# Optimization experiments

Hardware: AMD Instinct MI355X
Metric: run time of the kernel (lower is better)

Reference implementation:

```python
import jax, jax.numpy as jnp
import numpy as np

NUM_EXPERTS = 8
D_MODEL = 1024
HIDDEN = 3 * D_MODEL
TOP_K = 2
LAMBDA = 0.01


def setup_inputs() -> dict:
    key = jax.random.key(0)
    k_x, k_w1, k_w2, k_r = jax.random.split(key, 4)
    B, T, C = 4, 2048, D_MODEL
    x = jax.random.normal(k_x, (B, T, C), dtype=jnp.float32)
    # per-expert SwishFFN weights (bias=False): W1 [E, C, H], W2 [E, H, C]
    W1 = jax.random.normal(k_w1, (NUM_EXPERTS, C, HIDDEN), dtype=jnp.float32) * (1.0 / np.sqrt(C))
    W2 = jax.random.normal(k_w2, (NUM_EXPERTS, HIDDEN, C), dtype=jnp.float32) * (1.0 / np.sqrt(HIDDEN))
    # router projection [C, E]
    Wr = jax.random.normal(k_r, (C, NUM_EXPERTS), dtype=jnp.float32) * (1.0 / np.sqrt(C))
    return {"x": x, "W1": W1, "W2": W2, "Wr": Wr}


def reference(x, W1, W2, Wr):
    B, T, C = x.shape
    E = W1.shape[0]
    xf = x.reshape(-1, C)                       # [N, C], N = B*T
    N = xf.shape[0]

    # Router: softmax over experts, keep top-k, renormalize among the k
    logits = xf @ Wr                            # [N, E]
    all_probs = jax.nn.softmax(logits, axis=-1)
    vals, idx = jax.lax.top_k(all_probs, TOP_K)  # [N, K]
    vals = vals / jnp.sum(vals, axis=-1, keepdims=True)
    routing_weight = jnp.zeros((N, E), dtype=xf.dtype).at[
        jnp.arange(N)[:, None], idx
    ].set(vals)                                  # sparse [N, E]

    # Expert combine: sum_e w_e * FFN_e(x); w_e == 0 for non-selected tokens,
    # so this equals the original masked gather/scatter loop exactly.
    out = jnp.zeros_like(xf)
    for e in range(E):
        h = jax.nn.silu(xf @ W1[e])              # [N, H]
        out = out + routing_weight[:, e:e + 1] * (h @ W2[e])

    # Load-balancing aux loss (fi detached)
    fi = jax.lax.stop_gradient(
        jnp.mean((routing_weight > 0).astype(xf.dtype), axis=0))
    pi = jnp.mean(all_probs, axis=0)
    aux_loss = LAMBDA * E * jnp.sum(fi * pi)

    return out.reshape(B, T, C), aux_loss
```

## Files before the change

### kernel.cpp

```cpp
#include <hip/hip_runtime.h>
#include <stdint.h>

#define N_TOK 8192
#define C_DIM 1024
#define H_DIM 3072
#define N_EXP 8
#define N_ASSIGN (N_TOK * 2)

typedef __attribute__((ext_vector_type(8))) short short8;
typedef __attribute__((ext_vector_type(4))) float f32x4;

__device__ __forceinline__ unsigned short f2bf(float f) {
    union { float f; uint32_t u; } v; v.f = f;
    uint32_t r = (v.u + 0x7FFFu + ((v.u >> 16) & 1u)) >> 16;
    return (unsigned short)r;
}

#define GLDS16(SRC, DST) __builtin_amdgcn_global_load_lds( \
    (const __attribute__((address_space(1))) void*)(SRC),  \
    (__attribute__((address_space(3))) void*)(DST), 16, 0, 0)

#define SBAR() do { __builtin_amdgcn_sched_barrier(0); \
    __builtin_amdgcn_s_barrier();                      \
    __builtin_amdgcn_sched_barrier(0); } while (0)

#define VM_WAIT(S) do { __builtin_amdgcn_sched_barrier(0); \
    asm volatile(S ::: "memory");                          \
    __builtin_amdgcn_sched_barrier(0); } while (0)

__global__ __launch_bounds__(256) void transpose_bf16_kernel(const float* __restrict__ in,
                                                             unsigned short* __restrict__ out,
                                                             int rows, int cols) {
    __shared__ float tile[64][65];
    int e = blockIdx.z;
    const float* ip = in + (size_t)e * rows * cols;
    unsigned short* op = out + (size_t)e * rows * cols;
    int c0 = blockIdx.x * 64;
    int r0 = blockIdx.y * 64;
    int t = threadIdx.x;
    int lr = t >> 4, lc4 = t & 15;
#pragma unroll
    for (int it = 0; it < 4; it++) {
        int r = lr + it * 16;
        float4 v = *(const float4*)&ip[(size_t)(r0 + r) * cols + c0 + lc4 * 4];
        tile[lc4 * 4 + 0][r] = v.x;
        tile[lc4 * 4 + 1][r] = v.y;
        tile[lc4 * 4 + 2][r] = v.z;
        tile[lc4 * 4 + 3][r] = v.w;
    }
    __syncthreads();
#pragma unroll
    for (int it = 0; it < 4; it++) {
        int oc = lr + it * 16;
        ushort4 o;
        o.x = f2bf(tile[oc][lc4 * 4 + 0]);
        o.y = f2bf(tile[oc][lc4 * 4 + 1]);
        o.z = f2bf(tile[oc][lc4 * 4 + 2]);
        o.w = f2bf(tile[oc][lc4 * 4 + 3]);
        *(ushort4*)&op[(size_t)(c0 + oc) * rows + r0 + lc4 * 4] = o;
    }
}

__global__ __launch_bounds__(256) void router_kernel(const float* __restrict__ x, const float* __restrict__ Wr,
                                                     int2* __restrict__ idx2, float2* __restrict__ wgt2,
                                                     float* __restrict__ piAcc, int* __restrict__ cntAcc) {
    __shared__ float s_pi[8];
    __shared__ int s_cnt[8];
    int t = threadIdx.x;
    if (t < 8) { s_pi[t] = 0.f; s_cnt[t] = 0; }
    __syncthreads();
    int lane = t & 63;
    int wid = t >> 6;
    int gwv = blockIdx.x * 4 + wid;
    int nw = gridDim.x * 4;
    for (int n = gwv; n < N_TOK; n += nw) {
        float acc[8];
#pragma unroll
        for (int e = 0; e < 8; e++) acc[e] = 0.f;
        const float* xr = x + (size_t)n * C_DIM;
#pragma unroll
        for (int j = 0; j < 16; j++) {
            int k = lane + 64 * j;
            float xv = xr[k];
            const float4* wr4 = (const float4*)(Wr + (size_t)k * 8);
            float4 a = wr4[0], b = wr4[1];
            acc[0] += xv * a.x; acc[1] += xv * a.y; acc[2] += xv * a.z; acc[3] += xv * a.w;
            acc[4] += xv * b.x; acc[5] += xv * b.y; acc[6] += xv * b.z; acc[7] += xv * b.w;
        }
#pragma unroll
        for (int off = 1; off < 64; off <<= 1) {
#pragma unroll
            for (int e = 0; e < 8; e++) acc[e] += __shfl_xor(acc[e], off, 64);
        }
        float m = acc[0];
#pragma unroll
        for (int e = 1; e < 8; e++) m = fmaxf(m, acc[e]);
        float p[8]; float s = 0.f;
#pragma unroll
        for (int e = 0; e < 8; e++) { p[e] = __expf(acc[e] - m); s += p[e]; }
        float inv = 1.f / s;
#pragma unroll
        for (int e = 0; e < 8; e++) p[e] *= inv;
        int i0 = 0; float l0 = acc[0];
#pragma unroll
        for (int e = 1; e < 8; e++) if (acc[e] > l0) { l0 = acc[e]; i0 = e; }
        int i1 = -1; float l1 = -1e30f;
#pragma unroll
        for (int e = 0; e < 8; e++) if (e != i0 && acc[e] > l1) { l1 = acc[e]; i1 = e; }
        if (lane == 0) {
            float v0 = p[i0], v1 = p[i1];
            float rs = 1.f / (v0 + v1);
            idx2[n] = make_int2(i0, i1);
            wgt2[n] = make_float2(v0 * rs, v1 * rs);
            atomicAdd(&s_cnt[i0], 1);
            atomicAdd(&s_cnt[i1], 1);
#pragma unroll
            for (int e = 0; e < 8; e++) atomicAdd(&s_pi[e], p[e]);
        }
    }
    __syncthreads();
    if (t < 8) { atomicAdd(&piAcc[t], s_pi[t]); atomicAdd(&cntAcc[t], s_cnt[t]); }
}

__global__ void finalize_router_kernel(const int* __restrict__ cnt, const float* __restrict__ pi,
                                       int* __restrict__ off, float* __restrict__ aux_out) {
    if (threadIdx.x == 0) {
        int o = 0;
        float dot = 0.f;
        for (int e = 0; e < 8; e++) {
            off[e] = o;
            o += cnt[e];
            dot += (float)cnt[e] * pi[e];
        }
        aux_out[0] = 0.01f * 8.f * dot / ((float)N_TOK * (float)N_TOK);
    }
}

__global__ __launch_bounds__(256) void scatter_kernel(const int2* __restrict__ idx2, const float2* __restrict__ wgt2,
                                                      const int* __restrict__ off, int* __restrict__ cursor,
                                                      int* __restrict__ tok, float* __restrict__ gwArr) {
    __shared__ int lcnt[8], lbase[8];
    int t = threadIdx.x;
    if (t < 8) lcnt[t] = 0;
    __syncthreads();
    int a = blockIdx.x * 256 + t;
    int n = a >> 1, k = a & 1;
    int2 id = idx2[n];
    float2 w = wgt2[n];
    int e = k ? id.y : id.x;
    float wv = k ? w.y : w.x;
    int rank = atomicAdd(&lcnt[e], 1);
    __syncthreads();
    if (t < 8) lbase[t] = atomicAdd(&cursor[t], lcnt[t]);
    __syncthreads();
    int pos = off[e] + lbase[e] + rank;
    tok[pos] = n;
    gwArr[pos] = wv;
}

__global__ __launch_bounds__(256) void gather_kernel(const float* __restrict__ x, const int* __restrict__ tok,
                                                     unsigned short* __restrict__ xg) {
    int wid = threadIdx.x >> 6, lane = threadIdx.x & 63;
    int row = blockIdx.x * 4 + wid;
    int n = tok[row];
    const float4* src = (const float4*)(x + (size_t)n * C_DIM);
    ushort4* dst = (ushort4*)(xg + (size_t)row * C_DIM);
#pragma unroll
    for (int j = 0; j < 4; j++) {
        float4 v = src[lane + 64 * j];
        ushort4 o;
        o.x = f2bf(v.x); o.y = f2bf(v.y); o.z = f2bf(v.z); o.w = f2bf(v.w);
        dst[lane + 64 * j] = o;
    }
}

template <int EPI>
__global__ __launch_bounds__(512) void moe_gemm_kernel(
    const unsigned short* __restrict__ A, int ldA,
    const unsigned short* __restrict__ Bt, int ldB, int bRowOff, int bColOff,
    int Kseg, int NY, int SK,
    const int* __restrict__ cnt, const int* __restrict__ off,
    const int* __restrict__ tok, const float* __restrict__ gwArr,
    unsigned short* __restrict__ hs, int ldH,
    float* __restrict__ out) {
    __shared__ unsigned short smem[65536];

    int nbs[8];
    int tot = 0;
#pragma unroll
    for (int i = 0; i < 8; i++) {
        nbs[i] = (cnt[i] + 255) >> 8;
        tot += nbs[i] * NY * SK;
    }
    int p = blockIdx.x;
    int q = tot >> 3, r = tot & 7;
    int xx = p & 7, sp = p >> 3;
    int capx = (xx < r) ? q + 1 : q;
    if (sp >= capx) return;
    int wi = (xx < r) ? xx * (q + 1) + sp : r * (q + 1) + (xx - r) * q + sp;

    int base = 0, e = -1, enb = 0, local = 0;
#pragma unroll
    for (int i = 0; i < 8; i++) {
        int sz = nbs[i] * NY * SK;
        if (e < 0 && wi < base + sz) { e = i; enb = nbs[i]; local = wi - base; }
        base += sz;
    }
    if (e < 0) return;
    int ys = local / enb;
    int mblk = local - ys * enb;
    int s = ys / NY;
    int y = ys - s * NY;
    int M = cnt[e];
    int m0 = mblk * 256;
    int baseRow = off[e];
    int n0 = y * 256;
    int acol = s * Kseg;
    int bcol = bColOff + s * Kseg;

    int tid = threadIdx.x;
    int lane = tid & 63;
    int wid = tid >> 6;
    int wm = (wid >> 2) * 128;
    int wn = (wid & 3) * 64;

    f32x4 acc[8][4];
#pragma unroll
    for (int i = 0; i < 8; i++)
#pragma unroll
        for (int j = 0; j < 4; j++) acc[i][j] = (f32x4)0.f;

    const unsigned short* Bex = Bt + (size_t)e * (size_t)(C_DIM * H_DIM);

    const unsigned short* srcA[2];
    const unsigned short* srcB[2];
    int ldsOff[2];
#pragma unroll
    for (int i = 0; i < 2; i++) {
        int c = i * 512 + tid;
        int row = c >> 2;
        int pos = c & 3;
        int sc = pos ^ ((row >> 1) & 3);
        int rg = m0 + row; if (rg > M - 1) rg = M - 1;
        srcA[i] = A + (size_t)(baseRow + rg) * ldA + acol + sc * 8;
        srcB[i] = Bex + (size_t)(bRowOff + n0 + row) * ldB + bcol + sc * 8;
        ldsOff[i] = (c & ~63) * 8;
    }

    int kq = lane >> 4;
    int rsub = lane & 15;
    int offA[8], offB[4];
#pragma unroll
    for (int m = 0; m < 8; m++) {
        int rr = wm + m * 16 + rsub;
        offA[m] = rr * 32 + ((kq ^ ((rr >> 1) & 3)) * 8);
    }
#pragma unroll
    for (int n = 0; n < 4; n++) {
        int rn = wn + n * 16 + rsub;
        offB[n] = 8192 + rn * 32 + ((kq ^ ((rn >> 1) & 3)) * 8);
    }

    int nt = Kseg >> 5;
#pragma unroll
    for (int tt = 0; tt < 3; tt++) {
#pragma unroll
        for (int i = 0; i < 2; i++) GLDS16(srcA[i], &smem[tt * 16384 + ldsOff[i]]);
#pragma unroll
        for (int i = 0; i < 2; i++) GLDS16(srcB[i], &smem[tt * 16384 + 8192 + ldsOff[i]]);
#pragma unroll
        for (int i = 0; i < 2; i++) { srcA[i] += 32; srcB[i] += 32; }
    }

#pragma unroll 1
    for (int t = 0; t < nt; ++t) {
        if (t < nt - 2)      VM_WAIT("s_waitcnt vmcnt(8)");
        else if (t == nt - 2) VM_WAIT("s_waitcnt vmcnt(4)");
        else                 VM_WAIT("s_waitcnt vmcnt(0)");
        SBAR();
        const unsigned short* buf = &smem[(t & 3) * 16384];
        short8 a[8], b[4];
#pragma unroll
        for (int m = 0; m < 8; m++) a[m] = *(const short8*)&buf[offA[m]];
#pragma unroll
        for (int n = 0; n < 4; n++) b[n] = *(const short8*)&buf[offB[n]];
        if (t + 3 < nt) {
            int bb = ((t + 3) & 3) * 16384;
#pragma unroll
            for (int i = 0; i < 2; i++) GLDS16(srcA[i], &smem[bb + ldsOff[i]]);
#pragma unroll
            for (int i = 0; i < 2; i++) GLDS16(srcB[i], &smem[bb + 8192 + ldsOff[i]]);
#pragma unroll
            for (int i = 0; i < 2; i++) { srcA[i] += 32; srcB[i] += 32; }
        }
        __builtin_amdgcn_s_setprio(1);
#pragma unroll
        for (int m = 0; m < 8; m++)
#pragma unroll
            for (int n = 0; n < 4; n++)
                acc[m][n] = __builtin_amdgcn_mfma_f32_16x16x32_bf16(a[m], b[n], acc[m][n], 0, 0, 0);
        __builtin_amdgcn_s_setprio(0);
    }

    int gRow = (lane >> 4) * 4;
    int cLane = lane & 15;
#pragma unroll
    for (int m = 0; m < 8; m++) {
#pragma unroll
        for (int j = 0; j < 4; j++) {
            int rr = m0 + wm + m * 16 + gRow + j;
            if (rr < M) {
                if (EPI == 0) {
#pragma unroll
                    for (int n = 0; n < 4; n++) {
                        int c = n0 + wn + n * 16 + cLane;
                        float v = acc[m][n][j];
                        float sv = v / (1.f + __expf(-v));
                        hs[(size_t)(baseRow + rr) * ldH + c] = f2bf(sv);
                    }
                } else {
                    int token = tok[baseRow + rr];
                    float w = gwArr[baseRow + rr];
#pragma unroll
                    for (int n = 0; n < 4; n++) {
                        int c = n0 + wn + n * 16 + cLane;
                        atomicAdd(&out[(size_t)token * C_DIM + c], w * acc[m][n][j]);
                    }
                }
            }
        }
    }
}

extern "C" void kernel_launch(void* const* d_in, const int* in_sizes, int n_in,
                              void* d_out, int out_size, void* d_ws, size_t ws_size,
                              hipStream_t stream) {
    const float* x = (const float*)d_in[0];
    const float* W1 = (const float*)d_in[1];
    const float* W2 = (const float*)d_in[2];
    const float* Wr = (const float*)d_in[3];
    float* out = (float*)d_out;

    char* p = (char*)d_ws;
    auto alloc = [&](size_t bytes) {
        char* r = p;
        p += (bytes + 255) & ~(size_t)255;
        return r;
    };
    float* pi = (float*)alloc(8 * sizeof(float));
    int* cntA = (int*)alloc(8 * sizeof(int));
    int* cursor = (int*)alloc(8 * sizeof(int));
    int* offA = (int*)alloc(8 * sizeof(int));
    int2* idx2 = (int2*)alloc((size_t)N_TOK * sizeof(int2));
    float2* wgt2 = (float2*)alloc((size_t)N_TOK * sizeof(float2));
    int* tok = (int*)alloc((size_t)N_ASSIGN * sizeof(int));
    float* gwA = (float*)alloc((size_t)N_ASSIGN * sizeof(float));
    unsigned short* W1bT = (unsigned short*)alloc((size_t)N_EXP * C_DIM * H_DIM * 2);
    unsigned short* W2bT = (unsigned short*)alloc((size_t)N_EXP * C_DIM * H_DIM * 2);
    unsigned short* xg = (unsigned short*)alloc((size_t)N_ASSIGN * C_DIM * 2);
    size_t used = (size_t)(p - (char*)d_ws);
    size_t remain = ws_size > used ? ws_size - used : 0;
    int HC = H_DIM;
    while (HC > 768 && (size_t)N_ASSIGN * HC * 2 > remain) HC >>= 1;
    unsigned short* hs = (unsigned short*)p;

    hipMemsetAsync(d_ws, 0, 1024, stream);
    hipMemsetAsync(d_out, 0, (size_t)N_TOK * C_DIM * sizeof(float), stream);

    transpose_bf16_kernel<<<dim3(H_DIM / 64, C_DIM / 64, N_EXP), 256, 0, stream>>>(W1, W1bT, C_DIM, H_DIM);
    transpose_bf16_kernel<<<dim3(C_DIM / 64, H_DIM / 64, N_EXP), 256, 0, stream>>>(W2, W2bT, H_DIM, C_DIM);

    router_kernel<<<256, 256, 0, stream>>>(x, Wr, idx2, wgt2, pi, cntA);
    finalize_router_kernel<<<1, 64, 0, stream>>>(cntA, pi, offA, out + (size_t)N_TOK * C_DIM);
    scatter_kernel<<<N_ASSIGN / 256, 256, 0, stream>>>(idx2, wgt2, offA, cursor, tok, gwA);
    gather_kernel<<<N_ASSIGN / 4, 256, 0, stream>>>(x, tok, xg);

    int nChunks = H_DIM / HC;
    for (int ci = 0; ci < nChunks; ++ci) {
        int h0 = ci * HC;
        int ny1 = HC / 256;
        int sk2 = (HC % 768 == 0) ? 3 : 2;
        moe_gemm_kernel<0><<<dim3(71 * ny1 + 8, 1, 1), 512, 0, stream>>>(
            xg, C_DIM, W1bT, C_DIM, h0, 0, C_DIM, ny1, 1,
            cntA, offA, tok, gwA, hs, HC, out);
        moe_gemm_kernel<1><<<dim3(71 * 4 * sk2 + 8, 1, 1), 512, 0, stream>>>(
            hs, HC, W2bT, H_DIM, 0, h0, HC / sk2, 4, sk2,
            cntA, offA, tok, gwA, hs, HC, out);
    }
}
```

Measured before the change: 506.7 us.

## Retile MoE GEMM to 256x128 with BK=64 triple buffer and interleaved loads

Shrinks the per-block output tile from 256x256 to 256x128 and doubles the K step to 64. The pipeline moves to a 3-stage LDS ring with an 8-chunk XOR swizzle. Global-to-LDS loads are split into pieces interleaved between four MFMA phases, separated by barriers and explicit lgkmcnt waits. The aim is better overlap of memory and MFMA work, fewer LDS bank conflicts, and more blocks for load balancing. The cost is lower arithmetic intensity per block (more B/A reloads), more barriers per iteration, and a changed split-K factor for the second GEMM.

```diff
diff --git a/kernel.cpp b/kernel.cpp
--- a/kernel.cpp
+++ b/kernel.cpp
@@ -24,7 +24,7 @@
     __builtin_amdgcn_s_barrier();                      \
     __builtin_amdgcn_sched_barrier(0); } while (0)
 
-#define VM_WAIT(S) do { __builtin_amdgcn_sched_barrier(0); \
+#define WAITASM(S) do { __builtin_amdgcn_sched_barrier(0); \
     asm volatile(S ::: "memory");                          \
     __builtin_amdgcn_sched_barrier(0); } while (0)
 
@@ -183,7 +183,7 @@
     const int* __restrict__ tok, const float* __restrict__ gwArr,
     unsigned short* __restrict__ hs, int ldH,
     float* __restrict__ out) {
-    __shared__ unsigned short smem[65536];
+    __shared__ unsigned short smem[73728];
 
     int nbs[8];
     int tot = 0;
@@ -214,92 +214,165 @@
     int M = cnt[e];
     int m0 = mblk * 256;
     int baseRow = off[e];
-    int n0 = y * 256;
+    int n0 = y * 128;
     int acol = s * Kseg;
     int bcol = bColOff + s * Kseg;
 
     int tid = threadIdx.x;
     int lane = tid & 63;
     int wid = tid >> 6;
-    int wm = (wid >> 2) * 128;
-    int wn = (wid & 3) * 64;
-
-    f32x4 acc[8][4];
+    int wr = wid >> 2;
+    int wc = wid & 3;
+
+    f32x4 acc[8][2];
 #pragma unroll
     for (int i = 0; i < 8; i++)
 #pragma unroll
-        for (int j = 0; j < 4; j++) acc[i][j] = (f32x4)0.f;
+        for (int j = 0; j < 2; j++) acc[i][j] = (f32x4)0.f;
 
     const unsigned short* Bex = Bt + (size_t)e * (size_t)(C_DIM * H_DIM);
 
-    const unsigned short* srcA[2];
+    const unsigned short* srcA[4];
     const unsigned short* srcB[2];
-    int ldsOff[2];
+    int ldsA[4], ldsB[2];
+#pragma unroll
+    for (int i = 0; i < 4; i++) {
+        int c = i * 512 + tid;
+        int row = c >> 3;
+        int sc = (c & 7) ^ (row & 7);
+        int rg = m0 + row; if (rg > M - 1) rg = M - 1;
+        srcA[i] = A + (size_t)(baseRow + rg) * ldA + acol + sc * 8;
+        ldsA[i] = (c & ~63) * 8;
+    }
 #pragma unroll
     for (int i = 0; i < 2; i++) {
         int c = i * 512 + tid;
-        int row = c >> 2;
-        int pos = c & 3;
-        int sc = pos ^ ((row >> 1) & 3);
-        int rg = m0 + row; if (rg > M - 1) rg = M - 1;
-        srcA[i] = A + (size_t)(baseRow + rg) * ldA + acol + sc * 8;
+        int row = c >> 3;
+        int sc = (c & 7) ^ (row & 7);
         srcB[i] = Bex + (size_t)(bRowOff + n0 + row) * ldB + bcol + sc * 8;
-        ldsOff[i] = (c & ~63) * 8;
+        ldsB[i] = 16384 + (c & ~63) * 8;
     }
 
     int kq = lane >> 4;
     int rsub = lane & 15;
-    int offA[8], offB[4];
-#pragma unroll
-    for (int m = 0; m < 8; m++) {
-        int rr = wm + m * 16 + rsub;
-        offA[m] = rr * 32 + ((kq ^ ((rr >> 1) & 3)) * 8);
-    }
-#pragma unroll
-    for (int n = 0; n < 4; n++) {
-        int rn = wn + n * 16 + rsub;
-        offB[n] = 8192 + rn * 32 + ((kq ^ ((rn >> 1) & 3)) * 8);
-    }
-
-    int nt = Kseg >> 5;
-#pragma unroll
-    for (int tt = 0; tt < 3; tt++) {
-#pragma unroll
-        for (int i = 0; i < 2; i++) GLDS16(srcA[i], &smem[tt * 16384 + ldsOff[i]]);
-#pragma unroll
-        for (int i = 0; i < 2; i++) GLDS16(srcB[i], &smem[tt * 16384 + 8192 + ldsOff[i]]);
-#pragma unroll
-        for (int i = 0; i < 2; i++) { srcA[i] += 32; srcB[i] += 32; }
-    }
-
+    int offA[2][8], offB[2][2];
+#pragma unroll
+    for (int kk = 0; kk < 2; kk++) {
+#pragma unroll
+        for (int m = 0; m < 8; m++) {
+            int row = wr * 128 + m * 16 + rsub;
+            offA[kk][m] = row * 64 + (((kk * 4 + kq) ^ (row & 7)) * 8);
+        }
+#pragma unroll
+        for (int n = 0; n < 2; n++) {
+            int col = wc * 32 + n * 16 + rsub;
+            offB[kk][n] = 16384 + col * 64 + (((kk * 4 + kq) ^ (col & 7)) * 8);
+        }
+    }
+
+    int nt = Kseg >> 6;
+#pragma unroll
+    for (int tt = 0; tt < 2; tt++) {
+        int bb = tt * 24576;
+#pragma unroll
+        for (int i = 0; i < 4; i++) { GLDS16(srcA[i], &smem[bb + ldsA[i]]); srcA[i] += 64; }
+#pragma unroll
+        for (int i = 0; i < 2; i++) { GLDS16(srcB[i], &smem[bb + ldsB[i]]); srcB[i] += 64; }
+    }
+
+    int bufR = 0, bufW = 2 * 24576;
 #pragma unroll 1
     for (int t = 0; t < nt; ++t) {
-        if (t < nt - 2)      VM_WAIT("s_waitcnt vmcnt(8)");
-        else if (t == nt - 2) VM_WAIT("s_waitcnt vmcnt(4)");
-        else                 VM_WAIT("s_waitcnt vmcnt(0)");
-        SBAR();
-        const unsigned short* buf = &smem[(t & 3) * 16384];
-        short8 a[8], b[4];
-#pragma unroll
-        for (int m = 0; m < 8; m++) a[m] = *(const short8*)&buf[offA[m]];
-#pragma unroll
-        for (int n = 0; n < 4; n++) b[n] = *(const short8*)&buf[offB[n]];
-        if (t + 3 < nt) {
-            int bb = ((t + 3) & 3) * 16384;
-#pragma unroll
-            for (int i = 0; i < 2; i++) GLDS16(srcA[i], &smem[bb + ldsOff[i]]);
-#pragma unroll
-            for (int i = 0; i < 2; i++) GLDS16(srcB[i], &smem[bb + 8192 + ldsOff[i]]);
-#pragma unroll
-            for (int i = 0; i < 2; i++) { srcA[i] += 32; srcB[i] += 32; }
-        }
+        const unsigned short* bp = &smem[bufR];
+        bool ds = (t + 2 < nt);
+        short8 a0, a1, a2, a3, b0, b1;
+        if (ds) {
+            GLDS16(srcA[0], &smem[bufW + ldsA[0]]); srcA[0] += 64;
+            GLDS16(srcA[1], &smem[bufW + ldsA[1]]); srcA[1] += 64;
+        }
+        if (t < nt - 2)       WAITASM("s_waitcnt vmcnt(8)");
+        else if (t == nt - 2) WAITASM("s_waitcnt vmcnt(6)");
+        else                  WAITASM("s_waitcnt vmcnt(0)");
+        SBAR();
+        a0 = *(const short8*)&bp[offA[0][0]];
+        a1 = *(const short8*)&bp[offA[0][1]];
+        a2 = *(const short8*)&bp[offA[0][2]];
+        a3 = *(const short8*)&bp[offA[0][3]];
+        b0 = *(const short8*)&bp[offB[0][0]];
+        b1 = *(const short8*)&bp[offB[0][1]];
+        WAITASM("s_waitcnt lgkmcnt(0)");
         __builtin_amdgcn_s_setprio(1);
-#pragma unroll
-        for (int m = 0; m < 8; m++)
-#pragma unroll
-            for (int n = 0; n < 4; n++)
-                acc[m][n] = __builtin_amdgcn_mfma_f32_16x16x32_bf16(a[m], b[n], acc[m][n], 0, 0, 0);
+        acc[0][0] = __builtin_amdgcn_mfma_f32_16x16x32_bf16(a0, b0, acc[0][0], 0, 0, 0);
+        acc[0][1] = __builtin_amdgcn_mfma_f32_16x16x32_bf16(a0, b1, acc[0][1], 0, 0, 0);
+        acc[1][0] = __builtin_amdgcn_mfma_f32_16x16x32_bf16(a1, b0, acc[1][0], 0, 0, 0);
+        acc[1][1] = __builtin_amdgcn_mfma_f32_16x16x32_bf16(a1, b1, acc[1][1], 0, 0, 0);
+        acc[2][0] = __builtin_amdgcn_mfma_f32_16x16x32_bf16(a2, b0, acc[2][0], 0, 0, 0);
+        acc[2][1] = __builtin_amdgcn_mfma_f32_16x16x32_bf16(a2, b1, acc[2][1], 0, 0, 0);
+        acc[3][0] = __builtin_amdgcn_mfma_f32_16x16x32_bf16(a3, b0, acc[3][0], 0, 0, 0);
+        acc[3][1] = __builtin_amdgcn_mfma_f32_16x16x32_bf16(a3, b1, acc[3][1], 0, 0, 0);
         __builtin_amdgcn_s_setprio(0);
+        SBAR();
+        if (ds) {
+            GLDS16(srcA[2], &smem[bufW + ldsA[2]]); srcA[2] += 64;
+            GLDS16(srcA[3], &smem[bufW + ldsA[3]]); srcA[3] += 64;
+        }
+        a0 = *(const short8*)&bp[offA[0][4]];
+        a1 = *(const short8*)&bp[offA[0][5]];
+        a2 = *(const short8*)&bp[offA[0][6]];
+        a3 = *(const short8*)&bp[offA[0][7]];
+        SBAR();
+        WAITASM("s_waitcnt lgkmcnt(0)");
+        __builtin_amdgcn_s_setprio(1);
+        acc[4][0] = __builtin_amdgcn_mfma_f32_16x16x32_bf16(a0, b0, acc[4][0], 0, 0, 0);
+        acc[4][1] = __builtin_amdgcn_mfma_f32_16x16x32_bf16(a0, b1, acc[4][1], 0, 0, 0);
+        acc[5][0] = __builtin_amdgcn_mfma_f32_16x16x32_bf16(a1, b0, acc[5][0], 0, 0, 0);
+        acc[5][1] = __builtin_amdgcn_mfma_f32_16x16x32_bf16(a1, b1, acc[5][1], 0, 0, 0);
+        acc[6][0] = __builtin_amdgcn_mfma_f32_16x16x32_bf16(a2, b0, acc[6][0], 0, 0, 0);
+        acc[6][1] = __builtin_amdgcn_mfma_f32_16x16x32_bf16(a2, b1, acc[6][1], 0, 0, 0);
+        acc[7][0] = __builtin_amdgcn_mfma_f32_16x16x32_bf16(a3, b0, acc[7][0], 0, 0, 0);
+        acc[7][1] = __builtin_amdgcn_mfma_f32_16x16x32_bf16(a3, b1, acc[7][1], 0, 0, 0);
+        __builtin_amdgcn_s_setprio(0);
+        SBAR();
+        if (ds) { GLDS16(srcB[0], &smem[bufW + ldsB[0]]); srcB[0] += 64; }
+        a0 = *(const short8*)&bp[offA[1][0]];
+        a1 = *(const short8*)&bp[offA[1][1]];
+        a2 = *(const short8*)&bp[offA[1][2]];
+        a3 = *(const short8*)&bp[offA[1][3]];
+        b0 = *(const short8*)&bp[offB[1][0]];
+        b1 = *(const short8*)&bp[offB[1][1]];
+        SBAR();
+        WAITASM("s_waitcnt lgkmcnt(0)");
+        __builtin_amdgcn_s_setprio(1);
+        acc[0][0] = __builtin_amdgcn_mfma_f32_16x16x32_bf16(a0, b0, acc[0][0], 0, 0, 0);
+        acc[0][1] = __builtin_amdgcn_mfma_f32_16x16x32_bf16(a0, b1, acc[0][1], 0, 0, 0);
+        acc[1][0] = __builtin_amdgcn_mfma_f32_16x16x32_bf16(a1, b0, acc[1][0], 0, 0, 0);
+        acc[1][1] = __builtin_amdgcn_mfma_f32_16x16x32_bf16(a1, b1, acc[1][1], 0, 0, 0);
+        acc[2][0] = __builtin_amdgcn_mfma_f32_16x16x32_bf16(a2, b0, acc[2][0], 0, 0, 0);
+        acc[2][1] = __builtin_amdgcn_mfma_f32_16x16x32_bf16(a2, b1, acc[2][1], 0, 0, 0);
+        acc[3][0] = __builtin_amdgcn_mfma_f32_16x16x32_bf16(a3, b0, acc[3][0], 0, 0, 0);
+        acc[3][1] = __builtin_amdgcn_mfma_f32_16x16x32_bf16(a3, b1, acc[3][1], 0, 0, 0);
+        __builtin_amdgcn_s_setprio(0);
+        SBAR();
+        if (ds) { GLDS16(srcB[1], &smem[bufW + ldsB[1]]); srcB[1] += 64; }
+        a0 = *(const short8*)&bp[offA[1][4]];
+        a1 = *(const short8*)&bp[offA[1][5]];
+        a2 = *(const short8*)&bp[offA[1][6]];
+        a3 = *(const short8*)&bp[offA[1][7]];
+        SBAR();
+        WAITASM("s_waitcnt lgkmcnt(0)");
+        __builtin_amdgcn_s_setprio(1);
+        acc[4][0] = __builtin_amdgcn_mfma_f32_16x16x32_bf16(a0, b0, acc[4][0], 0, 0, 0);
+        acc[4][1] = __builtin_amdgcn_mfma_f32_16x16x32_bf16(a0, b1, acc[4][1], 0, 0, 0);
+        acc[5][0] = __builtin_amdgcn_mfma_f32_16x16x32_bf16(a1, b0, acc[5][0], 0, 0, 0);
+        acc[5][1] = __builtin_amdgcn_mfma_f32_16x16x32_bf16(a1, b1, acc[5][1], 0, 0, 0);
+        acc[6][0] = __builtin_amdgcn_mfma_f32_16x16x32_bf16(a2, b0, acc[6][0], 0, 0, 0);
+        acc[6][1] = __builtin_amdgcn_mfma_f32_16x16x32_bf16(a2, b1, acc[6][1], 0, 0, 0);
+        acc[7][0] = __builtin_amdgcn_mfma_f32_16x16x32_bf16(a3, b0, acc[7][0], 0, 0, 0);
+        acc[7][1] = __builtin_amdgcn_mfma_f32_16x16x32_bf16(a3, b1, acc[7][1], 0, 0, 0);
+        __builtin_amdgcn_s_setprio(0);
+        SBAR();
+        bufR += 24576; if (bufR == 73728) bufR = 0;
+        bufW += 24576; if (bufW == 73728) bufW = 0;
     }
 
     int gRow = (lane >> 4) * 4;
@@ -308,12 +381,12 @@
     for (int m = 0; m < 8; m++) {
 #pragma unroll
         for (int j = 0; j < 4; j++) {
-            int rr = m0 + wm + m * 16 + gRow + j;
+            int rr = m0 + wr * 128 + m * 16 + gRow + j;
             if (rr < M) {
                 if (EPI == 0) {
 #pragma unroll
-                    for (int n = 0; n < 4; n++) {
-                        int c = n0 + wn + n * 16 + cLane;
+                    for (int n = 0; n < 2; n++) {
+                        int c = n0 + wc * 32 + n * 16 + cLane;
                         float v = acc[m][n][j];
                         float sv = v / (1.f + __expf(-v));
                         hs[(size_t)(baseRow + rr) * ldH + c] = f2bf(sv);
@@ -322,8 +395,8 @@
                     int token = tok[baseRow + rr];
                     float w = gwArr[baseRow + rr];
 #pragma unroll
-                    for (int n = 0; n < 4; n++) {
-                        int c = n0 + wn + n * 16 + cLane;
+                    for (int n = 0; n < 2; n++) {
+                        int c = n0 + wc * 32 + n * 16 + cLane;
                         atomicAdd(&out[(size_t)token * C_DIM + c], w * acc[m][n][j]);
                     }
                 }
@@ -378,13 +451,13 @@
     int nChunks = H_DIM / HC;
     for (int ci = 0; ci < nChunks; ++ci) {
         int h0 = ci * HC;
-        int ny1 = HC / 256;
-        int sk2 = (HC % 768 == 0) ? 3 : 2;
+        int ny1 = HC / 128;
+        int sk2 = (HC >= 1536) ? 2 : 1;
         moe_gemm_kernel<0><<<dim3(71 * ny1 + 8, 1, 1), 512, 0, stream>>>(
             xg, C_DIM, W1bT, C_DIM, h0, 0, C_DIM, ny1, 1,
             cntA, offA, tok, gwA, hs, HC, out);
-        moe_gemm_kernel<1><<<dim3(71 * 4 * sk2 + 8, 1, 1), 512, 0, stream>>>(
-            hs, HC, W2bT, H_DIM, 0, h0, HC / sk2, 4, sk2,
+        moe_gemm_kernel<1><<<dim3(71 * 8 * sk2 + 8, 1, 1), 512, 0, stream>>>(
+            hs, HC, W2bT, H_DIM, 0, h0, HC / sk2, 8, sk2,
             cntA, offA, tok, gwA, hs, HC, out);
     }
 }
```

Measured after the change: 550.9 us. +8.7%, slower.
